# Kernel tuning notes

Hardware: AMD Instinct MI355X
Metric: run time of the kernel (lower is better)

Reference implementation:

```python
import jax, jax.numpy as jnp
import numpy as np

N_NODES = 50000
N_EDGES = 640000
IN_DIM = 128
HID = 128
OUT_DIM = 16
BATCH = 2
EPS = 1e-5


def setup_inputs() -> dict:
    key = jax.random.key(0)
    ks = jax.random.split(key, 12)
    x = jax.random.normal(ks[0], (BATCH, N_NODES, IN_DIM), dtype=jnp.float32)
    edge_index = jax.random.randint(ks[1], (2, N_EDGES), 0, N_NODES, dtype=jnp.int32)
    # learned per-edge log-weights (initialized ~0 like nn.Parameter(zeros), small noise for a nontrivial test)
    edge_weight_param = 0.01 * jax.random.normal(ks[2], (N_EDGES,), dtype=jnp.float32)
    s1 = 1.0 / np.sqrt(IN_DIM)
    s2 = 1.0 / np.sqrt(HID)
    W1 = jax.random.uniform(ks[3], (IN_DIM, HID), minval=-s1, maxval=s1, dtype=jnp.float32)
    b1 = jnp.zeros((HID,), jnp.float32)
    W2 = jax.random.uniform(ks[4], (HID, HID), minval=-s2, maxval=s2, dtype=jnp.float32)
    b2 = jnp.zeros((HID,), jnp.float32)
    g1 = jnp.ones((HID,), jnp.float32); be1 = jnp.zeros((HID,), jnp.float32)
    g2 = jnp.ones((HID,), jnp.float32); be2 = jnp.zeros((HID,), jnp.float32)
    Wc = jax.random.uniform(ks[5], (HID, OUT_DIM), minval=-s2, maxval=s2, dtype=jnp.float32)
    bc = jax.random.uniform(ks[6], (OUT_DIM,), minval=-s2, maxval=s2, dtype=jnp.float32)
    return {"x": x, "edge_index": edge_index, "edge_weight_param": edge_weight_param,
            "W1": W1, "b1": b1, "W2": W2, "b2": b2,
            "g1": g1, "be1": be1, "g2": g2, "be2": be2,
            "Wc": Wc, "bc": bc}


def _gcn_norm(edge_index, edge_weight):
    # PyG GCNConv: add self-loops (weight 1), symmetric D^-1/2 A D^-1/2 normalization
    row = jnp.concatenate([edge_index[0], jnp.arange(N_NODES, dtype=edge_index.dtype)])
    col = jnp.concatenate([edge_index[1], jnp.arange(N_NODES, dtype=edge_index.dtype)])
    ew = jnp.concatenate([edge_weight, jnp.ones((N_NODES,), edge_weight.dtype)])
    deg = jax.ops.segment_sum(ew, col, num_segments=N_NODES)
    dinv = jnp.where(deg > 0, jax.lax.rsqrt(jnp.maximum(deg, 1e-30)), 0.0)
    norm = dinv[row] * ew * dinv[col]
    return row, col, norm


def _gcn_conv(x, W, b, row, col, norm):
    # x: [B, N, F_in] -> [B, N, F_out]; gather-scale-scatter over edges
    xw = x @ W                                   # [B, N, H]
    msg = xw[:, row, :] * norm[None, :, None]    # [B, E+N, H]
    out = jax.vmap(lambda m: jax.ops.segment_sum(m, col, num_segments=N_NODES))(msg)
    return out + b


def _batchnorm(h, gamma, beta):
    # training-mode BN over flattened (B*N) rows, biased variance, eps=1e-5
    B, N, F = h.shape
    hf = h.reshape(-1, F)
    mu = hf.mean(axis=0)
    var = hf.var(axis=0)
    return (((hf - mu) * jax.lax.rsqrt(var + EPS)) * gamma + beta).reshape(B, N, F)


def reference(x, edge_index, edge_weight_param, W1, b1, W2, b2, g1, be1, g2, be2, Wc, bc):
    edge_weight = jnp.exp(edge_weight_param)  # learned exp edge weights
    row, col, norm = _gcn_norm(edge_index, edge_weight)
    h = jax.nn.relu(_gcn_conv(x, W1, b1, row, col, norm))
    h = _batchnorm(h, g1, be1)
    # dropout is identity in eval / deterministic reference
    h = jax.nn.relu(_gcn_conv(h, W2, b2, row, col, norm))
    h = _batchnorm(h, g2, be2)
    return h @ Wc + bc  # [B, N, OUT_DIM]
```

## Files before the change

kernel.cpp:

```cpp
#include <hip/hip_runtime.h>
#include <hip/hip_bf16.h>
#include <cstdint>
#include <cstddef>

#define N_NODES 50000
#define N_EDGES 640000
#define ROWS    100000
#define HID     128
#define OUTD    16
#define AGG_BLOCKS 2048
#define MID_BLOCKS 32
#define SCAN_BLOCKS 196
#define GEMM_BLOCKS 512
#define GEMM_TILES  (N_NODES / 8)
#define CLS_TILES   (ROWS / 16)

typedef __attribute__((ext_vector_type(8))) uint16_t ushort8;
typedef __attribute__((ext_vector_type(8))) __bf16   bf16x8;
typedef __attribute__((ext_vector_type(4))) float    floatx4;

union FragU { ushort8 u; bf16x8 b; };

__device__ __forceinline__ float bf_lo(uint32_t u){
  union { uint32_t u; float f; } c; c.u = u << 16; return c.f;
}
__device__ __forceinline__ float bf_hi(uint32_t u){
  union { uint32_t u; float f; } c; c.u = u & 0xffff0000u; return c.f;
}
__device__ __forceinline__ uint16_t f2bf(float f){
  union { float f; uint32_t u; } c; c.f = f;
  uint32_t u = c.u;
  uint32_t r = (u + 0x7fffu + ((u >> 16) & 1u)) >> 16;
  return (uint16_t)r;
}


__global__ void k_init(unsigned long long* __restrict__ dc){
  int i = blockIdx.x * 256 + threadIdx.x;
  if (i < N_NODES) dc[i] = 0ull;
}

__global__ void k_edge1(const int* __restrict__ ei, const float* __restrict__ ewp,
                        unsigned long long* __restrict__ dc, unsigned int* __restrict__ slot){
  int e = blockIdx.x * 256 + threadIdx.x;
  if (e < N_EDGES){
    float w = expf(ewp[e]);
    int c = ei[N_EDGES + e];
    unsigned long long inc = (1ull << 44) | (unsigned long long)(w * 1048576.0f + 0.5f);
    unsigned long long old = atomicAdd(&dc[c], inc);
    slot[e] = (unsigned int)(old >> 44);
  }
}

__global__ void k_scan_bsum(const unsigned long long* __restrict__ dc, int* __restrict__ bsum,
                            float* __restrict__ dinv){
  __shared__ int sd[256];
  int tid = threadIdx.x;
  int i = blockIdx.x * 256 + tid;
  int cnt = 0;
  if (i < N_NODES){
    unsigned long long v = dc[i];
    cnt = (int)(v >> 44);
    float deg = 1.0f + (float)((double)(v & ((1ull << 44) - 1)) * (1.0 / 1048576.0));
    dinv[i] = 1.0f / sqrtf(deg);
  }
  sd[tid] = cnt;
  __syncthreads();
  for (int off = 128; off > 0; off >>= 1){
    if (tid < off) sd[tid] += sd[tid + off];
    __syncthreads();
  }
  if (tid == 0) bsum[blockIdx.x] = sd[0];
}

__global__ void k_scan_excl(int* __restrict__ bsum){
  __shared__ int sd[256];
  int tid = threadIdx.x;
  sd[tid] = (tid < SCAN_BLOCKS) ? bsum[tid] : 0;
  __syncthreads();
  if (tid == 0){
    int run = 0;
    for (int i = 0; i < SCAN_BLOCKS; i++){ int t = sd[i]; sd[i] = run; run += t; }
  }
  __syncthreads();
  if (tid < SCAN_BLOCKS) bsum[tid] = sd[tid];
}

__global__ void k_scan_write(const unsigned long long* __restrict__ dc, const int* __restrict__ bsum,
                             int* __restrict__ rp){
  __shared__ int sd[256];
  int tid = threadIdx.x;
  int i = blockIdx.x * 256 + tid;
  int v = (i < N_NODES) ? (int)(dc[i] >> 44) : 0;
  sd[tid] = v;
  __syncthreads();
  for (int off = 1; off < 256; off <<= 1){
    int t = (tid >= off) ? sd[tid - off] : 0;
    __syncthreads();
    sd[tid] += t;
    __syncthreads();
  }
  if (i < N_NODES) rp[i] = bsum[blockIdx.x] + sd[tid] - v;
  if (blockIdx.x == 0 && tid == 0) rp[N_NODES] = N_EDGES;
}

__global__ void k_fill(const int* __restrict__ ei, const float* __restrict__ ewp,
                       const float* __restrict__ dinv, const unsigned int* __restrict__ slot,
                       const int* __restrict__ rp, unsigned long long* __restrict__ edg){
  int e = blockIdx.x * 256 + threadIdx.x;
  if (e < N_EDGES){
    int r = ei[e];
    int c = ei[N_EDGES + e];
    float w = expf(ewp[e]);
    float nrm = dinv[r] * w * dinv[c];
    int p = rp[c] + (int)slot[e];
    edg[p] = ((unsigned long long)__float_as_uint(nrm) << 32) | (unsigned int)r;
  }
}

__global__ void k_wpack(const float* __restrict__ W, const float* __restrict__ sca,
                        uint16_t* __restrict__ WP){
  int t = blockIdx.x * 256 + threadIdx.x;
  int L = t & 63;
  int s = (t >> 6) & 3;
  int c = t >> 8;
  int n = c * 16 + (L & 15);
  int k0 = s * 32 + (L >> 4) * 8;
  ushort8 r;
#pragma unroll
  for (int j = 0; j < 8; j++){
    float w = W[(size_t)(k0 + j) * HID + n];
    if (sca) w *= sca[k0 + j];
    r[j] = f2bf(w);
  }
  *((ushort8*)(WP + (size_t)t * 8)) = r;
}

__global__ void k_wpackc(const float* __restrict__ Wc, const float* __restrict__ sca,
                         uint16_t* __restrict__ WPC){
  int t = threadIdx.x;
  int L = t & 63;
  int s = t >> 6;
  int n = L & 15;
  int k0 = s * 32 + (L >> 4) * 8;
  ushort8 r;
#pragma unroll
  for (int j = 0; j < 8; j++)
    r[j] = f2bf(sca[k0 + j] * Wc[(size_t)(k0 + j) * OUTD + n]);
  *((ushort8*)(WPC + (size_t)t * 8)) = r;
}

__global__ void k_cvec(const float* __restrict__ shf, const float* __restrict__ W,
                       const float* __restrict__ bias, float* __restrict__ cv, int ncol, int stride){
  int j = threadIdx.x;
  if (j < ncol){
    float a = bias ? bias[j] : 0.f;
    for (int k = 0; k < HID; k++) a = fmaf(shf[k], W[(size_t)k * stride + j], a);
    cv[j] = a;
  }
}

template <bool FP32_IN>
__global__ __launch_bounds__(256, 2) void k_gemm_mfma(const void* __restrict__ Xv,
                                                      const uint16_t* __restrict__ WP,
                                                      uint16_t* __restrict__ Y){
  const int lane = threadIdx.x & 63;
  const int wid  = threadIdx.x >> 6;
  const int gw   = blockIdx.x * 4 + wid;
  const int nw   = GEMM_BLOCKS * 4;
  const int m    = lane & 15;
  const int kq   = lane >> 4;

  FragU wf[8][4];
#pragma unroll
  for (int c = 0; c < 8; c++)
#pragma unroll
    for (int s = 0; s < 4; s++)
      wf[c][s].u = *((const ushort8*)(WP + (size_t)(((c * 4 + s) * 64 + lane) * 8)));

  for (int t = gw; t < GEMM_TILES; t += nw){
    const int n0 = t * 8;
    const size_t ga = (size_t)((m & 1) * N_NODES + n0 + (m >> 1)) * HID;
    FragU af[4];
    if (FP32_IN){
      const float* X = (const float*)Xv;
#pragma unroll
      for (int s = 0; s < 4; s++){
        const float* p = X + ga + s * 32 + kq * 8;
        floatx4 f0 = *((const floatx4*)p);
        floatx4 f1 = *((const floatx4*)(p + 4));
        ushort8 r;
#pragma unroll
        for (int j = 0; j < 4; j++){ r[j] = f2bf(f0[j]); r[j + 4] = f2bf(f1[j]); }
        af[s].u = r;
      }
    } else {
      const uint16_t* X = (const uint16_t*)Xv;
#pragma unroll
      for (int s = 0; s < 4; s++)
        af[s].u = *((const ushort8*)(X + ga + s * 32 + kq * 8));
    }

    floatx4 acc[8];
#pragma unroll
    for (int c = 0; c < 8; c++) acc[c] = floatx4{0.f, 0.f, 0.f, 0.f};
#pragma unroll
    for (int s = 0; s < 4; s++)
#pragma unroll
      for (int c = 0; c < 8; c++)
        acc[c] = __builtin_amdgcn_mfma_f32_16x16x32_bf16(af[s].b, wf[c][s].b, acc[c], 0, 0, 0);

#pragma unroll
    for (int c = 0; c < 8; c++)
#pragma unroll
      for (int i = 0; i < 4; i++){
        int rr = kq * 4 + i;
        int node = n0 + (rr >> 1);
        int b = rr & 1;
        Y[(size_t)node * 256 + (size_t)(c * 8 + (m >> 1)) * 4 + b * 2 + (m & 1)] = f2bf(acc[c][i]);
      }
  }
}

__global__ __launch_bounds__(256) void k_cls_mfma(const uint16_t* __restrict__ H,
                                                  const uint16_t* __restrict__ WPC,
                                                  const float* __restrict__ cvec,
                                                  float* __restrict__ out){
  const int lane = threadIdx.x & 63;
  const int wid  = threadIdx.x >> 6;
  const int gw   = blockIdx.x * 4 + wid;
  const int nw   = GEMM_BLOCKS * 4;
  const int m    = lane & 15;
  const int kq   = lane >> 4;

  FragU wf[4];
#pragma unroll
  for (int s = 0; s < 4; s++)
    wf[s].u = *((const ushort8*)(WPC + (size_t)((s * 64 + lane) * 8)));
  const float cv = cvec[m];

  for (int t = gw; t < CLS_TILES; t += nw){
    const int row0 = t * 16;
    FragU af[4];
#pragma unroll
    for (int s = 0; s < 4; s++)
      af[s].u = *((const ushort8*)(H + (size_t)(row0 + m) * HID + s * 32 + kq * 8));
    floatx4 acc = floatx4{0.f, 0.f, 0.f, 0.f};
#pragma unroll
    for (int s = 0; s < 4; s++)
      acc = __builtin_amdgcn_mfma_f32_16x16x32_bf16(af[s].b, wf[s].b, acc, 0, 0, 0);
#pragma unroll
    for (int i = 0; i < 4; i++)
      out[(size_t)(row0 + kq * 4 + i) * OUTD + m] = acc[i] + cv;
  }
}

__global__ __launch_bounds__(256) void k_agg(const uint16_t* __restrict__ XW,
                                             const int* __restrict__ rp,
                                             const unsigned long long* __restrict__ edg,
                                             const float* __restrict__ dinv,
                                             const float* __restrict__ bias,
                                             const float* __restrict__ cvec,
                                             uint16_t* __restrict__ H,
                                             float* __restrict__ psum,
                                             float* __restrict__ pssq){
  __shared__ float lsum[128];
  __shared__ float lssq[128];
  const int tid = threadIdx.x;
  if (tid < 128){ lsum[tid] = 0.f; lssq[tid] = 0.f; }
  __syncthreads();

  const int lane = tid & 63;
  const int wid  = tid >> 6;
  const int gw   = blockIdx.x * 4 + wid;
  const int nw   = AGG_BLOCKS * 4;
  const uint32_t* Xu = (const uint32_t*)XW;
  uint32_t* Hu = (uint32_t*)H;
  const int f0 = lane * 2;
  const float b0 = bias[f0], b1 = bias[f0 + 1];
  const float c0 = cvec ? cvec[f0] : 0.f;
  const float c1 = cvec ? cvec[f0 + 1] : 0.f;
  float ts0 = 0.f, ts1 = 0.f, tq0 = 0.f, tq1 = 0.f;

  for (int node = gw; node < N_NODES; node += nw){
    const float di = dinv[node];
    const float sn = di * di;
    const int e0 = rp[node], e1 = rp[node + 1];
    uint2 sp = *((const uint2*)(Xu + (size_t)node * 128 + lane * 2));
    float a0x = sn * bf_lo(sp.x), a0y = sn * bf_hi(sp.x);
    float a1x = sn * bf_lo(sp.y), a1y = sn * bf_hi(sp.y);
    float wsum = sn;
    int e = e0;
    for (; e + 8 <= e1; e += 8){
      unsigned long long rec[8];
#pragma unroll
      for (int u = 0; u < 8; u++) rec[u] = edg[e + u];
      uint2 q[8];
#pragma unroll
      for (int u = 0; u < 8; u++){
        size_t src = (uint32_t)rec[u];
        q[u] = *((const uint2*)(Xu + src * 128 + lane * 2));
      }
#pragma unroll
      for (int u = 0; u < 8; u++){
        float w = __uint_as_float((uint32_t)(rec[u] >> 32));
        a0x = fmaf(w, bf_lo(q[u].x), a0x); a0y = fmaf(w, bf_hi(q[u].x), a0y);
        a1x = fmaf(w, bf_lo(q[u].y), a1x); a1y = fmaf(w, bf_hi(q[u].y), a1y);
        wsum += w;
      }
    }
    for (; e + 4 <= e1; e += 4){
      unsigned long long rec[4];
#pragma unroll
      for (int u = 0; u < 4; u++) rec[u] = edg[e + u];
      uint2 q[4];
#pragma unroll
      for (int u = 0; u < 4; u++){
        size_t src = (uint32_t)rec[u];
        q[u] = *((const uint2*)(Xu + src * 128 + lane * 2));
      }
#pragma unroll
      for (int u = 0; u < 4; u++){
        float w = __uint_as_float((uint32_t)(rec[u] >> 32));
        a0x = fmaf(w, bf_lo(q[u].x), a0x); a0y = fmaf(w, bf_hi(q[u].x), a0y);
        a1x = fmaf(w, bf_lo(q[u].y), a1x); a1y = fmaf(w, bf_hi(q[u].y), a1y);
        wsum += w;
      }
    }
    for (; e < e1; e++){
      unsigned long long rec = edg[e];
      size_t src = (uint32_t)rec;
      float w = __uint_as_float((uint32_t)(rec >> 32));
      uint2 q = *((const uint2*)(Xu + src * 128 + lane * 2));
      a0x = fmaf(w, bf_lo(q.x), a0x); a0y = fmaf(w, bf_hi(q.x), a0y);
      a1x = fmaf(w, bf_lo(q.y), a1x); a1y = fmaf(w, bf_hi(q.y), a1y);
      wsum += w;
    }
    a0x = fmaxf(fmaf(wsum, c0, a0x) + b0, 0.f); a0y = fmaxf(fmaf(wsum, c1, a0y) + b1, 0.f);
    a1x = fmaxf(fmaf(wsum, c0, a1x) + b0, 0.f); a1y = fmaxf(fmaf(wsum, c1, a1y) + b1, 0.f);
    Hu[(size_t)node * 64 + lane]             = (uint32_t)f2bf(a0x) | ((uint32_t)f2bf(a0y) << 16);
    Hu[(size_t)(N_NODES + node) * 64 + lane] = (uint32_t)f2bf(a1x) | ((uint32_t)f2bf(a1y) << 16);
    ts0 += a0x + a1x; ts1 += a0y + a1y;
    tq0 += a0x * a0x + a1x * a1x; tq1 += a0y * a0y + a1y * a1y;
  }

  atomicAdd(&lsum[f0],     ts0); atomicAdd(&lsum[f0 + 1], ts1);
  atomicAdd(&lssq[f0],     tq0); atomicAdd(&lssq[f0 + 1], tq1);
  __syncthreads();
  if (tid < 128){
    psum[(size_t)blockIdx.x * 128 + tid] = lsum[tid];
    pssq[(size_t)blockIdx.x * 128 + tid] = lssq[tid];
  }
}

__global__ __launch_bounds__(256) void k_bnmid(const float* __restrict__ psum,
                                               const float* __restrict__ pssq,
                                               float* __restrict__ msum,
                                               float* __restrict__ mssq){
  __shared__ float ss[2][128];
  __shared__ float sq[2][128];
  const int tid = threadIdx.x;
  const int f  = tid & 127;
  const int sl = tid >> 7;
  const int rows_per = AGG_BLOCKS / MID_BLOCKS;
  const int base = blockIdx.x * rows_per;
  float s = 0.f, q = 0.f;
  for (int r = base + sl; r < base + rows_per; r += 2){
    s += psum[(size_t)r * 128 + f];
    q += pssq[(size_t)r * 128 + f];
  }
  ss[sl][f] = s; sq[sl][f] = q;
  __syncthreads();
  if (tid < 128){
    msum[(size_t)blockIdx.x * 128 + tid] = ss[0][tid] + ss[1][tid];
    mssq[(size_t)blockIdx.x * 128 + tid] = sq[0][tid] + sq[1][tid];
  }
}

__global__ __launch_bounds__(128) void k_bnfin(const float* __restrict__ msum,
                                               const float* __restrict__ mssq,
                                               const float* __restrict__ gamma,
                                               const float* __restrict__ beta,
                                               float* __restrict__ sca,
                                               float* __restrict__ shf){
  const int f = threadIdx.x;
  float S = 0.f, Q = 0.f;
#pragma unroll
  for (int b = 0; b < MID_BLOCKS; b++){
    S += msum[(size_t)b * 128 + f];
    Q += mssq[(size_t)b * 128 + f];
  }
  const float inv = 1.0f / (float)ROWS;
  float mu = S * inv;
  float var = fmaxf(Q * inv - mu * mu, 0.f);
  float rstd = 1.0f / sqrtf(var + 1e-5f);
  float sc = gamma[f] * rstd;
  sca[f] = sc;
  shf[f] = fmaf(-mu, sc, beta[f]);
}

extern "C" void kernel_launch(void* const* d_in, const int* in_sizes, int n_in,
                              void* d_out, int out_size, void* d_ws, size_t ws_size,
                              hipStream_t stream){
  const float* x   = (const float*)d_in[0];
  const int*   ei  = (const int*)d_in[1];
  const float* ewp = (const float*)d_in[2];
  const float* W1  = (const float*)d_in[3];
  const float* b1  = (const float*)d_in[4];
  const float* W2  = (const float*)d_in[5];
  const float* b2  = (const float*)d_in[6];
  const float* g1  = (const float*)d_in[7];
  const float* be1 = (const float*)d_in[8];
  const float* g2  = (const float*)d_in[9];
  const float* be2 = (const float*)d_in[10];
  const float* Wc  = (const float*)d_in[11];
  const float* bc  = (const float*)d_in[12];
  float* out = (float*)d_out;

  char* wsb = (char*)d_ws;
  size_t off = 0;
  auto give = [&](size_t bytes) -> void* {
    void* p = wsb + off;
    off = (off + bytes + 255) & ~(size_t)255;
    return p;
  };
  uint16_t* XW  = (uint16_t*)give((size_t)ROWS * 128 * 2);
  uint16_t* Hb  = (uint16_t*)give((size_t)ROWS * 128 * 2);
  unsigned long long* DC  = (unsigned long long*)give((size_t)N_NODES * 8);
  unsigned long long* EDG = (unsigned long long*)give((size_t)N_EDGES * 8);
  unsigned int* SLOT = (unsigned int*)give((size_t)N_EDGES * 4);
  float* DINV   = (float*)give((size_t)N_NODES * 4);
  int*   RP     = (int*)give((size_t)(N_NODES + 1) * 4);
  int*   BSUM   = (int*)give(1024);
  float* PSUM   = (float*)give((size_t)AGG_BLOCKS * 128 * 4);
  float* PSSQ   = (float*)give((size_t)AGG_BLOCKS * 128 * 4);
  float* MSUM   = (float*)give((size_t)MID_BLOCKS * 128 * 4);
  float* MSSQ   = (float*)give((size_t)MID_BLOCKS * 128 * 4);
  float* SCA1   = (float*)give(512);
  float* SHF1   = (float*)give(512);
  float* SCA2   = (float*)give(512);
  float* SHF2   = (float*)give(512);
  uint16_t* WP1 = (uint16_t*)give((size_t)HID * HID * 2);
  uint16_t* WP2 = (uint16_t*)give((size_t)HID * HID * 2);
  uint16_t* WPC = (uint16_t*)give((size_t)HID * OUTD * 2);
  float* C2     = (float*)give(512);
  float* CVC    = (float*)give(64);
  (void)ws_size; (void)n_in; (void)in_sizes; (void)out_size;

  const int nb_nodes = (N_NODES + 255) / 256;
  const int nb_edges = (N_EDGES + 255) / 256;

  k_init<<<nb_nodes, 256, 0, stream>>>(DC);
  k_edge1<<<nb_edges, 256, 0, stream>>>(ei, ewp, DC, SLOT);
  k_scan_bsum<<<SCAN_BLOCKS, 256, 0, stream>>>(DC, BSUM, DINV);
  k_scan_excl<<<1, 256, 0, stream>>>(BSUM);
  k_scan_write<<<SCAN_BLOCKS, 256, 0, stream>>>(DC, BSUM, RP);
  k_fill<<<nb_edges, 256, 0, stream>>>(ei, ewp, DINV, SLOT, RP, EDG);
  k_wpack<<<8, 256, 0, stream>>>(W1, nullptr, WP1);

  k_gemm_mfma<true><<<GEMM_BLOCKS, 256, 0, stream>>>(x, WP1, XW);
  k_agg<<<AGG_BLOCKS, 256, 0, stream>>>(XW, RP, EDG, DINV, b1, nullptr, Hb, PSUM, PSSQ);
  k_bnmid<<<MID_BLOCKS, 256, 0, stream>>>(PSUM, PSSQ, MSUM, MSSQ);
  k_bnfin<<<1, 128, 0, stream>>>(MSUM, MSSQ, g1, be1, SCA1, SHF1);

  k_wpack<<<8, 256, 0, stream>>>(W2, SCA1, WP2);
  k_cvec<<<1, 128, 0, stream>>>(SHF1, W2, nullptr, C2, HID, HID);
  k_gemm_mfma<false><<<GEMM_BLOCKS, 256, 0, stream>>>(Hb, WP2, XW);
  k_agg<<<AGG_BLOCKS, 256, 0, stream>>>(XW, RP, EDG, DINV, b2, C2, Hb, PSUM, PSSQ);
  k_bnmid<<<MID_BLOCKS, 256, 0, stream>>>(PSUM, PSSQ, MSUM, MSSQ);
  k_bnfin<<<1, 128, 0, stream>>>(MSUM, MSSQ, g2, be2, SCA2, SHF2);

  k_wpackc<<<1, 256, 0, stream>>>(Wc, SCA2, WPC);
  k_cvec<<<1, 128, 0, stream>>>(SHF2, Wc, bc, CVC, OUTD, OUTD);
  k_cls_mfma<<<GEMM_BLOCKS, 256, 0, stream>>>(Hb, WPC, CVC, out);
}
```

Baseline: 378.9 us.

## Use batch-separated XW layout and aggregate per (node,batch) unit with 16-edge unroll

The GEMM output changes from an interleaved [node][feature][batch] layout to a plain row-major [batch*node][feature] layout. The aggregation kernel now gives each wave one (node, batch) unit, gathering 4-byte rows per lane instead of 8-byte interleaved pairs, and unrolls the edge loop to 16 gathers in flight. The aim is more memory-level parallelism and simpler indexing. The cost is that each edge record and its degree data are read twice, once per batch, and each gather moves half as much data per request, which increases the number of gather transactions.

Result: slower. 438.5 us (+15.7%).

```diff
diff --git a/kernel.cpp b/kernel.cpp
--- a/kernel.cpp
+++ b/kernel.cpp
@@ -12,8 +12,8 @@
 #define MID_BLOCKS 32
 #define SCAN_BLOCKS 196
 #define GEMM_BLOCKS 512
-#define GEMM_TILES  (N_NODES / 8)
-#define CLS_TILES   (ROWS / 16)
+#define GEMM_TILES  (ROWS / 16)
+#define AGG_UNITS   (2 * N_NODES)
 
 typedef __attribute__((ext_vector_type(8))) uint16_t ushort8;
 typedef __attribute__((ext_vector_type(8))) __bf16   bf16x8;
@@ -33,7 +33,6 @@
   uint32_t r = (u + 0x7fffu + ((u >> 16) & 1u)) >> 16;
   return (uint16_t)r;
 }
-
 
 __global__ void k_init(unsigned long long* __restrict__ dc){
   int i = blockIdx.x * 256 + threadIdx.x;
@@ -179,14 +178,13 @@
       wf[c][s].u = *((const ushort8*)(WP + (size_t)(((c * 4 + s) * 64 + lane) * 8)));
 
   for (int t = gw; t < GEMM_TILES; t += nw){
-    const int n0 = t * 8;
-    const size_t ga = (size_t)((m & 1) * N_NODES + n0 + (m >> 1)) * HID;
+    const int row0 = t * 16;
     FragU af[4];
     if (FP32_IN){
       const float* X = (const float*)Xv;
 #pragma unroll
       for (int s = 0; s < 4; s++){
-        const float* p = X + ga + s * 32 + kq * 8;
+        const float* p = X + (size_t)(row0 + m) * HID + s * 32 + kq * 8;
         floatx4 f0 = *((const floatx4*)p);
         floatx4 f1 = *((const floatx4*)(p + 4));
         ushort8 r;
@@ -198,7 +196,7 @@
       const uint16_t* X = (const uint16_t*)Xv;
 #pragma unroll
       for (int s = 0; s < 4; s++)
-        af[s].u = *((const ushort8*)(X + ga + s * 32 + kq * 8));
+        af[s].u = *((const ushort8*)(X + (size_t)(row0 + m) * HID + s * 32 + kq * 8));
     }
 
     floatx4 acc[8];
@@ -213,12 +211,8 @@
 #pragma unroll
     for (int c = 0; c < 8; c++)
 #pragma unroll
-      for (int i = 0; i < 4; i++){
-        int rr = kq * 4 + i;
-        int node = n0 + (rr >> 1);
-        int b = rr & 1;
-        Y[(size_t)node * 256 + (size_t)(c * 8 + (m >> 1)) * 4 + b * 2 + (m & 1)] = f2bf(acc[c][i]);
-      }
+      for (int i = 0; i < 4; i++)
+        Y[(size_t)(row0 + kq * 4 + i) * HID + c * 16 + m] = f2bf(acc[c][i]);
   }
 }
 
@@ -239,7 +233,7 @@
     wf[s].u = *((const ushort8*)(WPC + (size_t)((s * 64 + lane) * 8)));
   const float cv = cvec[m];
 
-  for (int t = gw; t < CLS_TILES; t += nw){
+  for (int t = gw; t < GEMM_TILES; t += nw){
     const int row0 = t * 16;
     FragU af[4];
 #pragma unroll
@@ -282,30 +276,29 @@
   const float c1 = cvec ? cvec[f0 + 1] : 0.f;
   float ts0 = 0.f, ts1 = 0.f, tq0 = 0.f, tq1 = 0.f;
 
-  for (int node = gw; node < N_NODES; node += nw){
+  for (int unit = gw; unit < AGG_UNITS; unit += nw){
+    const int node = unit >> 1;
+    const int b    = unit & 1;
+    const size_t base = (size_t)b * N_NODES * 64;
     const float di = dinv[node];
     const float sn = di * di;
     const int e0 = rp[node], e1 = rp[node + 1];
-    uint2 sp = *((const uint2*)(Xu + (size_t)node * 128 + lane * 2));
-    float a0x = sn * bf_lo(sp.x), a0y = sn * bf_hi(sp.x);
-    float a1x = sn * bf_lo(sp.y), a1y = sn * bf_hi(sp.y);
+    uint32_t sp = Xu[base + (size_t)node * 64 + lane];
+    float ax = sn * bf_lo(sp), ay = sn * bf_hi(sp);
     float wsum = sn;
     int e = e0;
-    for (; e + 8 <= e1; e += 8){
-      unsigned long long rec[8];
-#pragma unroll
-      for (int u = 0; u < 8; u++) rec[u] = edg[e + u];
-      uint2 q[8];
-#pragma unroll
-      for (int u = 0; u < 8; u++){
-        size_t src = (uint32_t)rec[u];
-        q[u] = *((const uint2*)(Xu + src * 128 + lane * 2));
-      }
-#pragma unroll
-      for (int u = 0; u < 8; u++){
+    for (; e + 16 <= e1; e += 16){
+      unsigned long long rec[16];
+#pragma unroll
+      for (int u = 0; u < 16; u++) rec[u] = edg[e + u];
+      uint32_t q[16];
+#pragma unroll
+      for (int u = 0; u < 16; u++)
+        q[u] = Xu[base + (size_t)(uint32_t)rec[u] * 64 + lane];
+#pragma unroll
+      for (int u = 0; u < 16; u++){
         float w = __uint_as_float((uint32_t)(rec[u] >> 32));
-        a0x = fmaf(w, bf_lo(q[u].x), a0x); a0y = fmaf(w, bf_hi(q[u].x), a0y);
-        a1x = fmaf(w, bf_lo(q[u].y), a1x); a1y = fmaf(w, bf_hi(q[u].y), a1y);
+        ax = fmaf(w, bf_lo(q[u]), ax); ay = fmaf(w, bf_hi(q[u]), ay);
         wsum += w;
       }
     }
@@ -313,35 +306,29 @@
       unsigned long long rec[4];
 #pragma unroll
       for (int u = 0; u < 4; u++) rec[u] = edg[e + u];
-      uint2 q[4];
-#pragma unroll
-      for (int u = 0; u < 4; u++){
-        size_t src = (uint32_t)rec[u];
-        q[u] = *((const uint2*)(Xu + src * 128 + lane * 2));
-      }
+      uint32_t q[4];
+#pragma unroll
+      for (int u = 0; u < 4; u++)
+        q[u] = Xu[base + (size_t)(uint32_t)rec[u] * 64 + lane];
 #pragma unroll
       for (int u = 0; u < 4; u++){
         float w = __uint_as_float((uint32_t)(rec[u] >> 32));
-        a0x = fmaf(w, bf_lo(q[u].x), a0x); a0y = fmaf(w, bf_hi(q[u].x), a0y);
-        a1x = fmaf(w, bf_lo(q[u].y), a1x); a1y = fmaf(w, bf_hi(q[u].y), a1y);
+        ax = fmaf(w, bf_lo(q[u]), ax); ay = fmaf(w, bf_hi(q[u]), ay);
         wsum += w;
       }
     }
     for (; e < e1; e++){
       unsigned long long rec = edg[e];
-      size_t src = (uint32_t)rec;
       float w = __uint_as_float((uint32_t)(rec >> 32));
-      uint2 q = *((const uint2*)(Xu + src * 128 + lane * 2));
-      a0x = fmaf(w, bf_lo(q.x), a0x); a0y = fmaf(w, bf_hi(q.x), a0y);
-      a1x = fmaf(w, bf_lo(q.y), a1x); a1y = fmaf(w, bf_hi(q.y), a1y);
+      uint32_t g = Xu[base + (size_t)(uint32_t)rec * 64 + lane];
+      ax = fmaf(w, bf_lo(g), ax); ay = fmaf(w, bf_hi(g), ay);
       wsum += w;
     }
-    a0x = fmaxf(fmaf(wsum, c0, a0x) + b0, 0.f); a0y = fmaxf(fmaf(wsum, c1, a0y) + b1, 0.f);
-    a1x = fmaxf(fmaf(wsum, c0, a1x) + b0, 0.f); a1y = fmaxf(fmaf(wsum, c1, a1y) + b1, 0.f);
-    Hu[(size_t)node * 64 + lane]             = (uint32_t)f2bf(a0x) | ((uint32_t)f2bf(a0y) << 16);
-    Hu[(size_t)(N_NODES + node) * 64 + lane] = (uint32_t)f2bf(a1x) | ((uint32_t)f2bf(a1y) << 16);
-    ts0 += a0x + a1x; ts1 += a0y + a1y;
-    tq0 += a0x * a0x + a1x * a1x; tq1 += a0y * a0y + a1y * a1y;
+    ax = fmaxf(fmaf(wsum, c0, ax) + b0, 0.f);
+    ay = fmaxf(fmaf(wsum, c1, ay) + b1, 0.f);
+    Hu[base + (size_t)node * 64 + lane] = (uint32_t)f2bf(ax) | ((uint32_t)f2bf(ay) << 16);
+    ts0 += ax; ts1 += ay;
+    tq0 += ax * ax; tq1 += ay * ay;
   }
 
   atomicAdd(&lsum[f0],     ts0); atomicAdd(&lsum[f0 + 1], ts1);
```
